# Optimization experiments

Measured on AMD Instinct MI355X. Metric: run time of the kernel, lower is better.

Reference implementation:

```python
import jax, jax.numpy as jnp
import numpy as np

N, M, D = 8192, 8192, 128
EPS = 1e-9


def setup_inputs() -> dict:
    key = jax.random.key(0)
    k1, k2 = jax.random.split(key)
    X = jax.random.normal(k1, (N, D), dtype=jnp.float32)
    Y = jax.random.normal(k2, (M, D), dtype=jnp.float32)
    sigma = jnp.ones((1,), dtype=jnp.float32)  # bandwidth (self.sigma)
    return {"X": X, "Y": Y, "sigma": sigma}


def reference(X, Y, sigma):
    # l2norm: ||x_i - y_j||^2 = ||x_i||^2 - 2 x_i.y_j + ||y_j||^2
    # (original builds full XX/YY Gram matrices just for their diagonals;
    #  same math via row-wise sums of squares)
    x2 = jnp.sum(X * X, axis=1)          # [n]
    y2 = jnp.sum(Y * Y, axis=1)          # [m]
    xy = jnp.matmul(X, Y.T)              # [n, m]
    dnorm2 = x2[:, None] - 2.0 * xy + y2[None, :]
    sigma2_inv = 1.0 / (sigma[0] ** 2 + EPS)
    K_XY = jnp.exp(-sigma2_inv * dnorm2)  # [n, m]
    return K_XY
```

## Files before the change

### kernel.cpp

```cpp
#include <hip/hip_runtime.h>
#include <stdint.h>

#define D_DIM 128
#define NROW 8192
#define MROW 8192
#define TILE 128
#define LDK 136
#define TLD 68
#define OUT_LD 8192

typedef __bf16 bf16x8 __attribute__((ext_vector_type(8)));
typedef float f32x4 __attribute__((ext_vector_type(4)));

union SMem {
    struct {
        unsigned short Xs[TILE][LDK];
        unsigned short Ys[TILE][LDK];
    } st;
    float tr[4][64 * TLD];
};

__device__ __forceinline__ unsigned short f32_to_bf16(float f) {
    uint32_t u = __float_as_uint(f);
    u = (u + 0x7FFFu + ((u >> 16) & 1u)) >> 16;
    return (unsigned short)u;
}

__global__ __launch_bounds__(256) void rbf_norms(const float* __restrict__ X,
                                                 const float* __restrict__ Y,
                                                 float* __restrict__ nrm) {
    const int t = threadIdx.x;
    const int w = t >> 6, lane = t & 63;
    const int rid = blockIdx.x * 4 + w;
    const float* src = (rid < NROW) ? (X + (size_t)rid * D_DIM)
                                    : (Y + (size_t)(rid - NROW) * D_DIM);
    float2 v = *(const float2*)(src + 2 * lane);
    float s = v.x * v.x + v.y * v.y;
    #pragma unroll
    for (int off = 32; off > 0; off >>= 1) s += __shfl_xor(s, off, 64);
    if (lane == 0) nrm[rid] = s;
}

__global__ __launch_bounds__(256) void rbf_main(const float* __restrict__ X,
                                                const float* __restrict__ Y,
                                                const float* __restrict__ sigma,
                                                const float* __restrict__ nrm,
                                                float* __restrict__ out) {
    __shared__ SMem sm;
    __shared__ float x2s[TILE];
    __shared__ float y2s[TILE];

    const int t = threadIdx.x;
    const int row0 = blockIdx.y * TILE;
    const int col0 = blockIdx.x * TILE;

    if (t < 128) x2s[t] = nrm[row0 + t];
    else         y2s[t - 128] = nrm[NROW + col0 + (t - 128)];

    #pragma unroll 4
    for (int i = 0; i < 16; ++i) {
        int f = t + 256 * i;
        int r = f >> 5;
        int q = (f & 31) * 4;
        float4 vx = *(const float4*)(X + (size_t)(row0 + r) * D_DIM + q);
        float4 vy = *(const float4*)(Y + (size_t)(col0 + r) * D_DIM + q);
        ushort4 hx = { f32_to_bf16(vx.x), f32_to_bf16(vx.y), f32_to_bf16(vx.z), f32_to_bf16(vx.w) };
        ushort4 hy = { f32_to_bf16(vy.x), f32_to_bf16(vy.y), f32_to_bf16(vy.z), f32_to_bf16(vy.w) };
        *(ushort4*)(&sm.st.Xs[r][q]) = hx;
        *(ushort4*)(&sm.st.Ys[r][q]) = hy;
    }
    __syncthreads();

    const int w = t >> 6, ln = t & 63;
    const int quad = ln >> 4, l16 = ln & 15;
    const int wr = (w >> 1) * 64;
    const int wc = (w & 1) * 64;

    f32x4 acc[4][4] = {};
    #pragma unroll
    for (int ks = 0; ks < 4; ++ks) {
        const int k = ks * 32 + quad * 8;
        bf16x8 a[4], b[4];
        #pragma unroll
        for (int ti = 0; ti < 4; ++ti)
            a[ti] = *(const bf16x8*)(&sm.st.Xs[wr + ti * 16 + l16][k]);
        #pragma unroll
        for (int tj = 0; tj < 4; ++tj)
            b[tj] = *(const bf16x8*)(&sm.st.Ys[wc + tj * 16 + l16][k]);
        #pragma unroll
        for (int ti = 0; ti < 4; ++ti)
            #pragma unroll
            for (int tj = 0; tj < 4; ++tj)
                acc[ti][tj] = __builtin_amdgcn_mfma_f32_16x16x32_bf16(a[ti], b[tj], acc[ti][tj], 0, 0, 0);
    }

    const float s2 = sigma[0] * sigma[0] + 1e-9f;
    const float cexp = -1.4426950408889634f / s2;

    __syncthreads();
    float* tw = sm.tr[w];
    #pragma unroll
    for (int ti = 0; ti < 4; ++ti)
        #pragma unroll
        for (int tj = 0; tj < 4; ++tj)
            #pragma unroll
            for (int r = 0; r < 4; ++r) {
                int lr = ti * 16 + quad * 4 + r;
                int lc = tj * 16 + l16;
                float d = x2s[wr + lr] + y2s[wc + lc] - 2.0f * acc[ti][tj][r];
                tw[lr * TLD + lc] = exp2f(d * cexp);
            }
    __syncthreads();

    #pragma unroll 4
    for (int i = 0; i < 16; ++i) {
        int lr = i * 4 + quad;
        f32x4 v = *(const f32x4*)(&tw[lr * TLD + l16 * 4]);
        size_t grow = (size_t)(row0 + wr + lr);
        size_t gcol = (size_t)(col0 + wc + l16 * 4);
        *(f32x4*)(out + grow * OUT_LD + gcol) = v;
    }
}

extern "C" void kernel_launch(void* const* d_in, const int* in_sizes, int n_in,
                              void* d_out, int out_size, void* d_ws, size_t ws_size,
                              hipStream_t stream) {
    const float* X = (const float*)d_in[0];
    const float* Y = (const float*)d_in[1];
    const float* sigma = (const float*)d_in[2];
    float* nrm = (float*)d_ws;
    float* out = (float*)d_out;

    rbf_norms<<<(NROW + MROW) / 4, 256, 0, stream>>>(X, Y, nrm);
    rbf_main<<<dim3(MROW / TILE, NROW / TILE), 256, 0, stream>>>(X, Y, sigma, nrm, out);
}
```

Measured before the change: 314.6 us.

## Swap MFMA operands for direct vector stores and halve LDS via K-split staging

The MFMA operands are swapped so each lane holds four consecutive output columns, which lets results be written straight to global memory as float4 non-temporal stores. This removes the LDS transpose buffer and its two barriers. The K dimension is staged in two halves of 64, cutting shared memory so that with launch_bounds(256,4) more blocks can be resident per CU. It also uses the raw hardware exp2 builtin. The costs are an extra barrier between the K halves and reduced exp2 accuracy or range handling.

```diff
diff --git a/kernel.cpp b/kernel.cpp
--- a/kernel.cpp
+++ b/kernel.cpp
@@ -5,20 +5,11 @@
 #define NROW 8192
 #define MROW 8192
 #define TILE 128
-#define LDK 136
-#define TLD 68
+#define LDK2 72
 #define OUT_LD 8192
 
 typedef __bf16 bf16x8 __attribute__((ext_vector_type(8)));
 typedef float f32x4 __attribute__((ext_vector_type(4)));
-
-union SMem {
-    struct {
-        unsigned short Xs[TILE][LDK];
-        unsigned short Ys[TILE][LDK];
-    } st;
-    float tr[4][64 * TLD];
-};
 
 __device__ __forceinline__ unsigned short f32_to_bf16(float f) {
     uint32_t u = __float_as_uint(f);
@@ -41,12 +32,13 @@
     if (lane == 0) nrm[rid] = s;
 }
 
-__global__ __launch_bounds__(256) void rbf_main(const float* __restrict__ X,
-                                                const float* __restrict__ Y,
-                                                const float* __restrict__ sigma,
-                                                const float* __restrict__ nrm,
-                                                float* __restrict__ out) {
-    __shared__ SMem sm;
+__global__ __launch_bounds__(256, 4) void rbf_main(const float* __restrict__ X,
+                                                   const float* __restrict__ Y,
+                                                   const float* __restrict__ sigma,
+                                                   const float* __restrict__ nrm,
+                                                   float* __restrict__ out) {
+    __shared__ unsigned short Xs[TILE][LDK2];
+    __shared__ unsigned short Ys[TILE][LDK2];
     __shared__ float x2s[TILE];
     __shared__ float y2s[TILE];
 
@@ -57,68 +49,70 @@
     if (t < 128) x2s[t] = nrm[row0 + t];
     else         y2s[t - 128] = nrm[NROW + col0 + (t - 128)];
 
-    #pragma unroll 4
-    for (int i = 0; i < 16; ++i) {
-        int f = t + 256 * i;
-        int r = f >> 5;
-        int q = (f & 31) * 4;
-        float4 vx = *(const float4*)(X + (size_t)(row0 + r) * D_DIM + q);
-        float4 vy = *(const float4*)(Y + (size_t)(col0 + r) * D_DIM + q);
-        ushort4 hx = { f32_to_bf16(vx.x), f32_to_bf16(vx.y), f32_to_bf16(vx.z), f32_to_bf16(vx.w) };
-        ushort4 hy = { f32_to_bf16(vy.x), f32_to_bf16(vy.y), f32_to_bf16(vy.z), f32_to_bf16(vy.w) };
-        *(ushort4*)(&sm.st.Xs[r][q]) = hx;
-        *(ushort4*)(&sm.st.Ys[r][q]) = hy;
-    }
-    __syncthreads();
-
     const int w = t >> 6, ln = t & 63;
     const int quad = ln >> 4, l16 = ln & 15;
     const int wr = (w >> 1) * 64;
     const int wc = (w & 1) * 64;
 
     f32x4 acc[4][4] = {};
+
     #pragma unroll
-    for (int ks = 0; ks < 4; ++ks) {
-        const int k = ks * 32 + quad * 8;
-        bf16x8 a[4], b[4];
+    for (int p = 0; p < 2; ++p) {
         #pragma unroll
-        for (int ti = 0; ti < 4; ++ti)
-            a[ti] = *(const bf16x8*)(&sm.st.Xs[wr + ti * 16 + l16][k]);
+        for (int i = 0; i < 8; ++i) {
+            int f = t + 256 * i;
+            int r = f >> 4;
+            int c = (f & 15) * 4;
+            float4 vx = *(const float4*)(X + (size_t)(row0 + r) * D_DIM + p * 64 + c);
+            float4 vy = *(const float4*)(Y + (size_t)(col0 + r) * D_DIM + p * 64 + c);
+            ushort4 hx = { f32_to_bf16(vx.x), f32_to_bf16(vx.y), f32_to_bf16(vx.z), f32_to_bf16(vx.w) };
+            ushort4 hy = { f32_to_bf16(vy.x), f32_to_bf16(vy.y), f32_to_bf16(vy.z), f32_to_bf16(vy.w) };
+            *(ushort4*)(&Xs[r][c]) = hx;
+            *(ushort4*)(&Ys[r][c]) = hy;
+        }
+        __syncthreads();
+
         #pragma unroll
-        for (int tj = 0; tj < 4; ++tj)
-            b[tj] = *(const bf16x8*)(&sm.st.Ys[wc + tj * 16 + l16][k]);
-        #pragma unroll
-        for (int ti = 0; ti < 4; ++ti)
+        for (int ks = 0; ks < 2; ++ks) {
+            const int k = ks * 32 + quad * 8;
+            bf16x8 ax[4], by[4];
+            #pragma unroll
+            for (int ti = 0; ti < 4; ++ti)
+                ax[ti] = *(const bf16x8*)(&Xs[wr + ti * 16 + l16][k]);
             #pragma unroll
             for (int tj = 0; tj < 4; ++tj)
-                acc[ti][tj] = __builtin_amdgcn_mfma_f32_16x16x32_bf16(a[ti], b[tj], acc[ti][tj], 0, 0, 0);
+                by[tj] = *(const bf16x8*)(&Ys[wc + tj * 16 + l16][k]);
+            #pragma unroll
+            for (int ti = 0; ti < 4; ++ti)
+                #pragma unroll
+                for (int tj = 0; tj < 4; ++tj)
+                    acc[ti][tj] = __builtin_amdgcn_mfma_f32_16x16x32_bf16(by[tj], ax[ti], acc[ti][tj], 0, 0, 0);
+        }
+        if (p == 0) __syncthreads();
     }
 
     const float s2 = sigma[0] * sigma[0] + 1e-9f;
     const float cexp = -1.4426950408889634f / s2;
 
-    __syncthreads();
-    float* tw = sm.tr[w];
+    float x2r[4];
     #pragma unroll
-    for (int ti = 0; ti < 4; ++ti)
+    for (int ti = 0; ti < 4; ++ti) x2r[ti] = x2s[wr + ti * 16 + l16];
+
+    #pragma unroll
+    for (int tj = 0; tj < 4; ++tj) {
+        f32x4 y2v = *(const f32x4*)(&y2s[wc + tj * 16 + quad * 4]);
+        size_t gcol = (size_t)(col0 + wc + tj * 16 + quad * 4);
         #pragma unroll
-        for (int tj = 0; tj < 4; ++tj)
+        for (int ti = 0; ti < 4; ++ti) {
+            f32x4 v;
             #pragma unroll
             for (int r = 0; r < 4; ++r) {
-                int lr = ti * 16 + quad * 4 + r;
-                int lc = tj * 16 + l16;
-                float d = x2s[wr + lr] + y2s[wc + lc] - 2.0f * acc[ti][tj][r];
-                tw[lr * TLD + lc] = exp2f(d * cexp);
+                float d = x2r[ti] + y2v[r] - 2.0f * acc[ti][tj][r];
+                v[r] = __builtin_amdgcn_exp2f(d * cexp);
             }
-    __syncthreads();
-
-    #pragma unroll 4
-    for (int i = 0; i < 16; ++i) {
-        int lr = i * 4 + quad;
-        f32x4 v = *(const f32x4*)(&tw[lr * TLD + l16 * 4]);
-        size_t grow = (size_t)(row0 + wr + lr);
-        size_t gcol = (size_t)(col0 + wc + l16 * 4);
-        *(f32x4*)(out + grow * OUT_LD + gcol) = v;
+            size_t grow = (size_t)(row0 + wr + ti * 16 + l16);
+            __builtin_nontemporal_store(v, (f32x4*)(out + grow * OUT_LD + gcol));
+        }
     }
 }
 
```

Result: no change. 309.2 us (-1.7%).
